# Kernel tuning notes

Measured on AMD Instinct MI355X. Metric: run time of the kernel, lower is better.

The kernel has to match this reference:

```python
import jax, jax.numpy as jnp
import numpy as np

NUM_LAYERS = 3
HEADS = 4
HEAD_DIM = 64
NUM_GRAPHS = 64


def setup_inputs() -> dict:
    key = jax.random.key(0)
    ks = jax.random.split(key, 12)
    N, E, C = 50000, 800000, HEADS * HEAD_DIM  # C = 256
    x = jax.random.normal(ks[0], (N, C), dtype=jnp.float32)
    edge_index = jax.random.randint(ks[1], (2, E), 0, N, dtype=jnp.int32)
    batch = jnp.sort(jax.random.randint(ks[2], (N,), 0, NUM_GRAPHS, dtype=jnp.int32))
    s = 1.0 / np.sqrt(C)
    Wq = jax.random.normal(ks[3], (NUM_LAYERS, C, C), dtype=jnp.float32) * s
    Wk = jax.random.normal(ks[4], (NUM_LAYERS, C, C), dtype=jnp.float32) * s
    Wv = jax.random.normal(ks[5], (NUM_LAYERS, C, C), dtype=jnp.float32) * s
    bq = jnp.zeros((NUM_LAYERS, C), dtype=jnp.float32)
    bk = jnp.zeros((NUM_LAYERS, C), dtype=jnp.float32)
    bv = jnp.zeros((NUM_LAYERS, C), dtype=jnp.float32)
    W1 = jax.random.normal(ks[6], (C, 64), dtype=jnp.float32) * s
    b1 = jnp.zeros((64,), dtype=jnp.float32)
    W2 = jax.random.normal(ks[7], (64, 16), dtype=jnp.float32) * (1.0 / 8.0)
    b2 = jnp.zeros((16,), dtype=jnp.float32)
    return {"x": x, "edge_index": edge_index, "batch": batch,
            "Wq": Wq, "bq": bq, "Wk": Wk, "bk": bk, "Wv": Wv, "bv": bv,
            "W1": W1, "b1": b1, "W2": W2, "b2": b2}


def _segment_softmax(scores, seg, num_segments):
    # scores: [E, H]; softmax over edges sharing the same destination node
    m = jax.ops.segment_max(scores, seg, num_segments=num_segments)
    e = jnp.exp(scores - m[seg])
    z = jax.ops.segment_sum(e, seg, num_segments=num_segments)
    return e / (z[seg] + 1e-16)


def reference(x, edge_index, batch, Wq, bq, Wk, bk, Wv, bv, W1, b1, W2, b2):
    N = x.shape[0]
    src, dst = edge_index[0], edge_index[1]
    scale = 1.0 / jnp.sqrt(jnp.asarray(HEAD_DIM, dtype=x.dtype))
    h = x
    for l in range(NUM_LAYERS):
        q = (h @ Wq[l] + bq[l]).reshape(N, HEADS, HEAD_DIM)
        k = (h @ Wk[l] + bk[l]).reshape(N, HEADS, HEAD_DIM)
        v = (h @ Wv[l] + bv[l]).reshape(N, HEADS, HEAD_DIM)
        # edge-wise attention logits: q_i . k_j / sqrt(d)  -> [E, H]
        alpha = jnp.einsum('ehd,ehd->eh', q[dst], k[src]) * scale
        alpha = _segment_softmax(alpha, dst, N)
        msg = alpha[..., None] * v[src]                     # [E, H, D]
        out = jax.ops.segment_sum(msg, dst, num_segments=N)  # [N, H, D]
        h = jax.nn.relu(out.reshape(N, HEADS * HEAD_DIM))
    # global add pool over graphs in the batch
    g = jax.ops.segment_sum(h, batch, num_segments=NUM_GRAPHS)  # [G, C]
    y = jax.nn.relu(g @ W1 + b1) @ W2 + b2                      # [G, 16]
    return y
```

## Files before the change

kernel.cpp:

```cpp
#include <hip/hip_runtime.h>
#include <math.h>

#define CC 256
#define HEADS 4
#define HD 64
#define NG 64
#define SCAN_BS 512
#define QKVS 768

typedef __attribute__((ext_vector_type(8))) _Float16 f16x8;
typedef __attribute__((ext_vector_type(4))) float f32x4;
typedef __attribute__((ext_vector_type(4))) _Float16 f16x4;
typedef __attribute__((ext_vector_type(2))) _Float16 f16x2;

static __device__ __forceinline__ float h2f(unsigned short u) {
  return (float)__builtin_bit_cast(_Float16, u);
}

#if __has_builtin(__builtin_amdgcn_fdot2)
static __device__ __forceinline__ float qkdot(f16x2 q0, f16x2 q1, f16x4 k) {
  f16x2 k0 = {k.x, k.y}, k1 = {k.z, k.w};
  return __builtin_amdgcn_fdot2(q0, k0, __builtin_amdgcn_fdot2(q1, k1, 0.f, false), false);
}
#else
static __device__ __forceinline__ float qkdot(f16x2 q0, f16x2 q1, f16x4 k) {
  return (float)q0.x * (float)k.x + (float)q0.y * (float)k.y +
         (float)q1.x * (float)k.z + (float)q1.y * (float)k.w;
}
#endif

static __device__ __forceinline__ int swz(int row, int g) {
  return row * 32 + (((g) ^ ((row >> 2) & 3)) << 3);
}

__global__ void prep_kernel(const int* __restrict__ dst, int* __restrict__ deg, int E,
                            const float* __restrict__ Wq, const float* __restrict__ Wk,
                            const float* __restrict__ Wv, const float* __restrict__ bq,
                            const float* __restrict__ bk, const float* __restrict__ bv,
                            unsigned short* __restrict__ Bth,
                            float* __restrict__ biascat, int L,
                            const float* __restrict__ x, unsigned short* __restrict__ hq,
                            int n4, int nbh, int nbw) {
  int b = blockIdx.x;
  if (b < nbh) {
    int e = b * 256 + threadIdx.x;
    if (e < E) atomicAdd(&deg[dst[e]], 1);
    return;
  }
  b -= nbh;
  if (b < nbw) {
    int idx = b * 256 + threadIdx.x;
    int total = L * QKVS * CC;
    if (idx >= total) return;
    int k = idx & 255;
    int n = (idx >> 8) % QKVS;
    int l = idx / (QKVS * CC);
    int part = n >> 8;
    int nn = n & 255;
    const float* W = part == 0 ? Wq : (part == 1 ? Wk : Wv);
    float v = W[((long)l * CC + k) * CC + nn];
    Bth[idx] = __builtin_bit_cast(unsigned short, (_Float16)v);
    if (k == 0) {
      const float* bb = part == 0 ? bq : (part == 1 ? bk : bv);
      biascat[l * QKVS + n] = bb[l * CC + nn];
    }
    return;
  }
  b -= nbw;
  int i = b * 256 + threadIdx.x;
  if (i >= n4) return;
  float4 v = ((const float4*)x)[i];
  ushort4 hv = make_ushort4(__builtin_bit_cast(unsigned short, (_Float16)v.x),
                            __builtin_bit_cast(unsigned short, (_Float16)v.y),
                            __builtin_bit_cast(unsigned short, (_Float16)v.z),
                            __builtin_bit_cast(unsigned short, (_Float16)v.w));
  ((ushort4*)hq)[i] = hv;
}

__global__ void scan1_kernel(const int* __restrict__ deg, int* __restrict__ exc,
                             int* __restrict__ partial, int n) {
  __shared__ int s[SCAN_BS];
  int t = threadIdx.x;
  int g = blockIdx.x * SCAN_BS + t;
  int v = (g < n) ? deg[g] : 0;
  s[t] = v;
  __syncthreads();
  for (int off = 1; off < SCAN_BS; off <<= 1) {
    int add = (t >= off) ? s[t - off] : 0;
    __syncthreads();
    s[t] += add;
    __syncthreads();
  }
  if (g < n) exc[g] = s[t] - v;
  if (t == SCAN_BS - 1) partial[blockIdx.x] = s[t];
}

__global__ void scan2_kernel(int* __restrict__ partial, int nb) {
  __shared__ int s[SCAN_BS];
  int t = threadIdx.x;
  int v = (t < nb) ? partial[t] : 0;
  s[t] = v;
  __syncthreads();
  for (int off = 1; off < SCAN_BS; off <<= 1) {
    int add = (t >= off) ? s[t - off] : 0;
    __syncthreads();
    s[t] += add;
    __syncthreads();
  }
  if (t < nb) partial[t] = s[t] - v;
}

__global__ void scan3_kernel(const int* __restrict__ exc, const int* __restrict__ partial,
                             int* __restrict__ row_start, int* __restrict__ cursor,
                             int n, int E) {
  int g = blockIdx.x * blockDim.x + threadIdx.x;
  if (g < n) {
    int v = exc[g] + partial[g / SCAN_BS];
    row_start[g] = v;
    cursor[g] = v;
  }
  if (g == n) row_start[n] = E;
}

__global__ void scatter_kernel(const int* __restrict__ srcArr, const int* __restrict__ dstArr,
                               int* __restrict__ cursor, int* __restrict__ csr_src, int E) {
  int e = blockIdx.x * blockDim.x + threadIdx.x;
  if (e < E) {
    int d = dstArr[e];
    int p = atomicAdd(&cursor[d], 1);
    csr_src[p] = srcArr[e];
  }
}

__global__ __launch_bounds__(256) void qkv_gemm(const unsigned short* __restrict__ Aq,
                                                const unsigned short* __restrict__ Bh,
                                                const float* __restrict__ biascat,
                                                _Float16* __restrict__ qkvh, int M,
                                                int nmb) {
  __shared__ unsigned short S[17408];
  unsigned short* As = S;
  unsigned short* Bs = S + 4096;
  int t = threadIdx.x;

  int G = 6 * nmb;
  int xcd = blockIdx.x & 7, pos = blockIdx.x >> 3;
  int q8 = G >> 3, r8 = G & 7;
  int lid = (xcd < r8 ? xcd * (q8 + 1) : r8 * (q8 + 1) + (xcd - r8) * q8) + pos;
  int bn = lid % 6, bm = lid / 6;

  int lane = t & 63, wave = t >> 6;
  int mo = (wave >> 1) * 64, no = (wave & 1) * 64;
  int col_l = lane & 15, q = lane >> 4;

  f32x4 acc[4][4];
#pragma unroll
  for (int i = 0; i < 4; ++i)
#pragma unroll
    for (int j = 0; j < 4; ++j) acc[i][j] = (f32x4)0.f;

  int sr = t >> 1;
  int sh = (t & 1) * 16;
  int g0 = (t & 1) * 2;
  int w0 = swz(sr, g0);
  int w1 = swz(sr, g0 + 1);
  long arow = (long)bm * 128 + sr;
  bool aval = arow < M;
  const unsigned short* ag = Aq + arow * CC + sh;
  const unsigned short* bg = Bh + ((long)bn * 128 + sr) * CC + sh;
  uint4 zz = make_uint4(0, 0, 0, 0);

  for (int kt = 0; kt < CC; kt += 32) {
    uint4 a0 = zz, a1 = zz;
    if (aval) {
      a0 = *(const uint4*)(ag + kt);
      a1 = *(const uint4*)(ag + kt + 8);
    }
    uint4 b0 = *(const uint4*)(bg + kt);
    uint4 b1 = *(const uint4*)(bg + kt + 8);
    __syncthreads();
    *(uint4*)&As[w0] = a0;
    *(uint4*)&As[w1] = a1;
    *(uint4*)&Bs[w0] = b0;
    *(uint4*)&Bs[w1] = b1;
    __syncthreads();

    f16x8 af[4], bf[4];
#pragma unroll
    for (int i = 0; i < 4; ++i) {
      int am = mo + i * 16 + col_l;
      af[i] = *(const f16x8*)&As[swz(am, q)];
      int bnn = no + i * 16 + col_l;
      bf[i] = *(const f16x8*)&Bs[swz(bnn, q)];
    }
#pragma unroll
    for (int i = 0; i < 4; ++i)
#pragma unroll
      for (int j = 0; j < 4; ++j)
        acc[i][j] = __builtin_amdgcn_mfma_f32_16x16x32_f16(af[i], bf[j], acc[i][j], 0, 0, 0);
  }

  long rbase = (long)bm * 128 + mo;
  int cbase = bn * 128 + no;
  __syncthreads();
  unsigned short* T = S + wave * 4352;
#pragma unroll
  for (int j = 0; j < 4; ++j) {
    int col = cbase + j * 16 + col_l;
    float bias = biascat[col];
    int cl = j * 16 + col_l;
#pragma unroll
    for (int i = 0; i < 4; ++i) {
#pragma unroll
      for (int r = 0; r < 4; ++r) {
        int rl = i * 16 + q * 4 + r;
        T[rl * 68 + cl] =
            __builtin_bit_cast(unsigned short, (_Float16)(acc[i][j][r] + bias));
      }
    }
  }
  __syncthreads();
  int ocol = cbase + (lane & 15) * 4;
#pragma unroll
  for (int p = 0; p < 16; ++p) {
    int rl = p * 4 + (lane >> 4);
    uint2 v = *(const uint2*)&T[rl * 68 + (lane & 15) * 4];
    long row = rbase + rl;
    if (row < M) *(uint2*)(qkvh + row * QKVS + ocol) = v;
  }
}

__global__ __launch_bounds__(256) void attn_fused_kernel(const _Float16* __restrict__ qkv,
                                                         const int* __restrict__ row_start,
                                                         const int* __restrict__ csr_src,
                                                         unsigned short* __restrict__ hq,
                                                         int N, int npx) {
  int b = blockIdx.x;
  int nb = (b & 7) * npx + (b >> 3);
  int wave = threadIdx.x >> 6;
  int lane = threadIdx.x & 63;
  int node = nb * 4 + wave;
  if (node >= N) return;
  int s0 = row_start[node], s1 = row_start[node + 1];

  const f16x4 q4 = *(const f16x4*)(qkv + (size_t)node * QKVS + lane * 4);
  const f16x2 q0 = {q4.x, q4.y};
  const f16x2 q1 = {q4.z, q4.w};

  float m = -1e30f, z = 0.f;
  f32x4 acc = (f32x4)0.f;

  int i = s0;
  for (; i + 8 <= s1; i += 8) {
    int ix[8];
#pragma unroll
    for (int u = 0; u < 8; ++u) ix[u] = csr_src[i + u];
    f16x4 kk[8], vv[8];
#pragma unroll
    for (int u = 0; u < 8; ++u) {
      const _Float16* rowp = qkv + (size_t)ix[u] * QKVS + 256 + lane * 4;
      kk[u] = *(const f16x4*)rowp;
      vv[u] = *(const f16x4*)(rowp + 256);
    }
    float lg[8];
#pragma unroll
    for (int u = 0; u < 8; ++u) {
      float d = qkdot(q0, q1, kk[u]);
#pragma unroll
      for (int off = 1; off < 16; off <<= 1) d += __shfl_xor(d, off, 64);
      lg[u] = d * 0.125f;
    }
    float cm = lg[0];
#pragma unroll
    for (int u = 1; u < 8; ++u) cm = fmaxf(cm, lg[u]);
    float mn = fmaxf(m, cm);
    float sc = __expf(m - mn);
    z *= sc;
    acc *= sc;
    m = mn;
#pragma unroll
    for (int u = 0; u < 8; ++u) {
      float e = __expf(lg[u] - m);
      z += e;
      f32x4 vf = {(float)vv[u].x, (float)vv[u].y, (float)vv[u].z, (float)vv[u].w};
      acc += e * vf;
    }
  }
  for (; i < s1; ++i) {
    int s = csr_src[i];
    const _Float16* rowp = qkv + (size_t)s * QKVS + 256 + lane * 4;
    f16x4 k4 = *(const f16x4*)rowp;
    f16x4 v4 = *(const f16x4*)(rowp + 256);
    float d = qkdot(q0, q1, k4);
#pragma unroll
    for (int off = 1; off < 16; off <<= 1) d += __shfl_xor(d, off, 64);
    float lgs = d * 0.125f;
    float mn = fmaxf(m, lgs);
    float sc = __expf(m - mn);
    float e = __expf(lgs - mn);
    z = z * sc + e;
    f32x4 vf = {(float)v4.x, (float)v4.y, (float)v4.z, (float)v4.w};
    acc = acc * sc + e * vf;
    m = mn;
  }

  float rz = 1.f / (z + 1e-16f);
  float o0 = fmaxf(acc.x * rz, 0.f);
  float o1 = fmaxf(acc.y * rz, 0.f);
  float o2 = fmaxf(acc.z * rz, 0.f);
  float o3 = fmaxf(acc.w * rz, 0.f);
  ushort4 ov = make_ushort4(__builtin_bit_cast(unsigned short, (_Float16)o0),
                            __builtin_bit_cast(unsigned short, (_Float16)o1),
                            __builtin_bit_cast(unsigned short, (_Float16)o2),
                            __builtin_bit_cast(unsigned short, (_Float16)o3));
  size_t idx = (size_t)node * CC + lane * 4;
  *(ushort4*)(hq + idx) = ov;
}

__global__ void pool_kernel(const unsigned short* __restrict__ hq,
                            const int* __restrict__ batch,
                            float* __restrict__ gpool, int N) {
  int c = threadIdx.x;
  int n0 = blockIdx.x * 64;
  int n1 = min(n0 + 64, N);
  int cur = batch[n0];
  float acc = 0.f;
  for (int n = n0; n < n1; ++n) {
    int g = batch[n];
    if (g != cur) {
      atomicAdd(&gpool[cur * CC + c], acc);
      acc = 0.f;
      cur = g;
    }
    acc += h2f(hq[(size_t)n * CC + c]);
  }
  atomicAdd(&gpool[cur * CC + c], acc);
}

__global__ void head_kernel(const float* __restrict__ gpool, const float* __restrict__ W1,
                            const float* __restrict__ b1, const float* __restrict__ W2,
                            const float* __restrict__ b2, float* __restrict__ out) {
  __shared__ float hid[64];
  int g = blockIdx.x, t = threadIdx.x;
  float acc = b1[t];
  for (int i = 0; i < CC; ++i) acc = fmaf(gpool[g * CC + i], W1[i * 64 + t], acc);
  hid[t] = fmaxf(acc, 0.f);
  __syncthreads();
  if (t < 16) {
    float o = b2[t];
    for (int i = 0; i < 64; ++i) o = fmaf(hid[i], W2[i * 16 + t], o);
    out[g * 16 + t] = o;
  }
}

extern "C" void kernel_launch(void* const* d_in, const int* in_sizes, int n_in,
                              void* d_out, int out_size, void* d_ws, size_t ws_size,
                              hipStream_t stream) {
  const float* x  = (const float*)d_in[0];
  const int* ei   = (const int*)d_in[1];
  const int* batch = (const int*)d_in[2];
  const float* Wq = (const float*)d_in[3];
  const float* bq = (const float*)d_in[4];
  const float* Wk = (const float*)d_in[5];
  const float* bk = (const float*)d_in[6];
  const float* Wv = (const float*)d_in[7];
  const float* bv = (const float*)d_in[8];
  const float* W1 = (const float*)d_in[9];
  const float* b1 = (const float*)d_in[10];
  const float* W2 = (const float*)d_in[11];
  const float* b2 = (const float*)d_in[12];
  float* out = (float*)d_out;

  int N = in_sizes[0] / CC;
  int E = in_sizes[1] / 2;
  int L = in_sizes[3] / (CC * CC);
  const int* src = ei;
  const int* dst = ei + E;

  size_t off = 0;
  auto alloc = [&](size_t bytes) -> void* {
    void* p = (char*)d_ws + off;
    off += (bytes + 255) & ~(size_t)255;
    return p;
  };
  _Float16* qkvh = (_Float16*)alloc((size_t)N * QKVS * 2);
  unsigned short* hq = (unsigned short*)alloc((size_t)N * CC * 2);
  unsigned short* Bth = (unsigned short*)alloc((size_t)L * QKVS * CC * 2);
  float* biascat = (float*)alloc((size_t)L * QKVS * 4);
  int* deg = (int*)alloc((size_t)N * 4);
  int* exc = (int*)alloc((size_t)N * 4);
  int* partial = (int*)alloc(SCAN_BS * 4);
  int* row_start = (int*)alloc((size_t)(N + 1) * 4);
  int* cursor = (int*)alloc((size_t)N * 4);
  int* csr_src = (int*)alloc((size_t)E * 4);
  float* gpool = (float*)alloc((size_t)NG * CC * 4);

  hipMemsetAsync(deg, 0, (size_t)N * 4, stream);
  int eb = (E + 255) / 256;
  int wtot = L * QKVS * CC;
  int nbw = (wtot + 255) / 256;
  int n4 = N * CC / 4;
  int nbs = (n4 + 255) / 256;
  prep_kernel<<<eb + nbw + nbs, 256, 0, stream>>>(dst, deg, E,
                                                  Wq, Wk, Wv, bq, bk, bv,
                                                  Bth, biascat, L,
                                                  x, hq, n4, eb, nbw);

  int nb = (N + SCAN_BS - 1) / SCAN_BS;
  scan1_kernel<<<nb, SCAN_BS, 0, stream>>>(deg, exc, partial, N);
  scan2_kernel<<<1, SCAN_BS, 0, stream>>>(partial, nb);
  scan3_kernel<<<(N + 1 + 255) / 256, 256, 0, stream>>>(exc, partial, row_start, cursor, N, E);
  scatter_kernel<<<eb, 256, 0, stream>>>(src, dst, cursor, csr_src, E);

  int nmb = (N + 127) / 128;
  int gemmG = 6 * nmb;
  int nblocks = (N + 3) / 4;
  int npx = (nblocks + 7) / 8;
  int ngrid = npx * 8;
  for (int l = 0; l < L; ++l) {
    qkv_gemm<<<gemmG, 256, 0, stream>>>(hq,
                                        Bth + (size_t)l * QKVS * CC,
                                        biascat + (size_t)l * QKVS, qkvh, N, nmb);
    attn_fused_kernel<<<ngrid, 256, 0, stream>>>(qkvh, row_start, csr_src,
                                                 hq, N, npx);
  }

  hipMemsetAsync(gpool, 0, (size_t)NG * CC * 4, stream);
  pool_kernel<<<(N + 63) / 64, 256, 0, stream>>>(hq, batch, gpool, N);
  head_kernel<<<NG, 64, 0, stream>>>(gpool, W1, b1, W2, b2, out);
}
```

Measured before the change: 694.9 us.

## Fuse graph pooling into last attention layer and widen GEMM K-tile

Global add pooling is folded into the final attention kernel. Each block stages its four node outputs in shared memory and atomically adds them into gpool, which removes the separate pool kernel and the fp16 write and re-read of h for the last layer. The gpool zeroing moves from a separate memset into the prep kernel. The QKV GEMM now loads K-tiles of 64 instead of 32, with a new 8-way XOR swizzle, halving the number of barriers. Its epilogue writes 16-byte stores instead of 8-byte ones and drops one barrier. The trade-off is many more global float atomics, all contending on the few gpool rows of the same graph, since the batch is sorted.

```diff
diff --git a/kernel.cpp b/kernel.cpp
--- a/kernel.cpp
+++ b/kernel.cpp
@@ -29,8 +29,8 @@
 }
 #endif
 
-static __device__ __forceinline__ int swz(int row, int g) {
-  return row * 32 + (((g) ^ ((row >> 2) & 3)) << 3);
+static __device__ __forceinline__ int swz64(int row, int g) {
+  return row * 64 + (((g) ^ ((row) & 7)) << 3);
 }
 
 __global__ void prep_kernel(const int* __restrict__ dst, int* __restrict__ deg, int E,
@@ -40,7 +40,8 @@
                             unsigned short* __restrict__ Bth,
                             float* __restrict__ biascat, int L,
                             const float* __restrict__ x, unsigned short* __restrict__ hq,
-                            int n4, int nbh, int nbw) {
+                            float* __restrict__ gpool,
+                            int n4, int nbh, int nbw, int nbs) {
   int b = blockIdx.x;
   if (b < nbh) {
     int e = b * 256 + threadIdx.x;
@@ -67,14 +68,20 @@
     return;
   }
   b -= nbw;
+  if (b < nbs) {
+    int i = b * 256 + threadIdx.x;
+    if (i >= n4) return;
+    float4 v = ((const float4*)x)[i];
+    ushort4 hv = make_ushort4(__builtin_bit_cast(unsigned short, (_Float16)v.x),
+                              __builtin_bit_cast(unsigned short, (_Float16)v.y),
+                              __builtin_bit_cast(unsigned short, (_Float16)v.z),
+                              __builtin_bit_cast(unsigned short, (_Float16)v.w));
+    ((ushort4*)hq)[i] = hv;
+    return;
+  }
+  b -= nbs;
   int i = b * 256 + threadIdx.x;
-  if (i >= n4) return;
-  float4 v = ((const float4*)x)[i];
-  ushort4 hv = make_ushort4(__builtin_bit_cast(unsigned short, (_Float16)v.x),
-                            __builtin_bit_cast(unsigned short, (_Float16)v.y),
-                            __builtin_bit_cast(unsigned short, (_Float16)v.z),
-                            __builtin_bit_cast(unsigned short, (_Float16)v.w));
-  ((ushort4*)hq)[i] = hv;
+  if (i < NG * CC) gpool[i] = 0.f;
 }
 
 __global__ void scan1_kernel(const int* __restrict__ deg, int* __restrict__ exc,
@@ -137,9 +144,9 @@
                                                 const float* __restrict__ biascat,
                                                 _Float16* __restrict__ qkvh, int M,
                                                 int nmb) {
-  __shared__ unsigned short S[17408];
+  __shared__ unsigned short S[18432];
   unsigned short* As = S;
-  unsigned short* Bs = S + 4096;
+  unsigned short* Bs = S + 8192;
   int t = threadIdx.x;
 
   int G = 6 * nmb;
@@ -159,50 +166,62 @@
     for (int j = 0; j < 4; ++j) acc[i][j] = (f32x4)0.f;
 
   int sr = t >> 1;
-  int sh = (t & 1) * 16;
-  int g0 = (t & 1) * 2;
-  int w0 = swz(sr, g0);
-  int w1 = swz(sr, g0 + 1);
+  int h = t & 1;
   long arow = (long)bm * 128 + sr;
   bool aval = arow < M;
-  const unsigned short* ag = Aq + arow * CC + sh;
-  const unsigned short* bg = Bh + ((long)bn * 128 + sr) * CC + sh;
+  const unsigned short* ag = Aq + arow * CC + h * 32;
+  const unsigned short* bg = Bh + ((long)bn * 128 + sr) * CC + h * 32;
   uint4 zz = make_uint4(0, 0, 0, 0);
-
-  for (int kt = 0; kt < CC; kt += 32) {
-    uint4 a0 = zz, a1 = zz;
+  int woff[4];
+#pragma unroll
+  for (int i = 0; i < 4; ++i) woff[i] = swz64(sr, h * 4 + i);
+
+  for (int kt = 0; kt < CC; kt += 64) {
+    uint4 a0 = zz, a1 = zz, a2 = zz, a3 = zz;
     if (aval) {
       a0 = *(const uint4*)(ag + kt);
       a1 = *(const uint4*)(ag + kt + 8);
+      a2 = *(const uint4*)(ag + kt + 16);
+      a3 = *(const uint4*)(ag + kt + 24);
     }
     uint4 b0 = *(const uint4*)(bg + kt);
     uint4 b1 = *(const uint4*)(bg + kt + 8);
-    __syncthreads();
-    *(uint4*)&As[w0] = a0;
-    *(uint4*)&As[w1] = a1;
-    *(uint4*)&Bs[w0] = b0;
-    *(uint4*)&Bs[w1] = b1;
-    __syncthreads();
-
-    f16x8 af[4], bf[4];
-#pragma unroll
-    for (int i = 0; i < 4; ++i) {
-      int am = mo + i * 16 + col_l;
-      af[i] = *(const f16x8*)&As[swz(am, q)];
-      int bnn = no + i * 16 + col_l;
-      bf[i] = *(const f16x8*)&Bs[swz(bnn, q)];
-    }
-#pragma unroll
-    for (int i = 0; i < 4; ++i)
-#pragma unroll
-      for (int j = 0; j < 4; ++j)
-        acc[i][j] = __builtin_amdgcn_mfma_f32_16x16x32_f16(af[i], bf[j], acc[i][j], 0, 0, 0);
+    uint4 b2 = *(const uint4*)(bg + kt + 16);
+    uint4 b3 = *(const uint4*)(bg + kt + 24);
+    __syncthreads();
+    *(uint4*)&As[woff[0]] = a0;
+    *(uint4*)&As[woff[1]] = a1;
+    *(uint4*)&As[woff[2]] = a2;
+    *(uint4*)&As[woff[3]] = a3;
+    *(uint4*)&Bs[woff[0]] = b0;
+    *(uint4*)&Bs[woff[1]] = b1;
+    *(uint4*)&Bs[woff[2]] = b2;
+    *(uint4*)&Bs[woff[3]] = b3;
+    __syncthreads();
+
+#pragma unroll
+    for (int kk = 0; kk < 64; kk += 32) {
+      int gb = (kk >> 3) + q;
+      f16x8 af[4], bf[4];
+#pragma unroll
+      for (int i = 0; i < 4; ++i) {
+        int am = mo + i * 16 + col_l;
+        af[i] = *(const f16x8*)&As[swz64(am, gb)];
+        int bnn = no + i * 16 + col_l;
+        bf[i] = *(const f16x8*)&Bs[swz64(bnn, gb)];
+      }
+#pragma unroll
+      for (int i = 0; i < 4; ++i)
+#pragma unroll
+        for (int j = 0; j < 4; ++j)
+          acc[i][j] = __builtin_amdgcn_mfma_f32_16x16x32_f16(af[i], bf[j], acc[i][j], 0, 0, 0);
+    }
   }
 
   long rbase = (long)bm * 128 + mo;
   int cbase = bn * 128 + no;
   __syncthreads();
-  unsigned short* T = S + wave * 4352;
+  unsigned short* T = S + wave * 4608;
 #pragma unroll
   for (int j = 0; j < 4; ++j) {
     int col = cbase + j * 16 + col_l;
@@ -213,19 +232,19 @@
 #pragma unroll
       for (int r = 0; r < 4; ++r) {
         int rl = i * 16 + q * 4 + r;
-        T[rl * 68 + cl] =
+        T[rl * 72 + cl] =
             __builtin_bit_cast(unsigned short, (_Float16)(acc[i][j][r] + bias));
       }
     }
   }
-  __syncthreads();
-  int ocol = cbase + (lane & 15) * 4;
-#pragma unroll
-  for (int p = 0; p < 16; ++p) {
-    int rl = p * 4 + (lane >> 4);
-    uint2 v = *(const uint2*)&T[rl * 68 + (lane & 15) * 4];
+  int c8 = (lane & 7) * 8;
+  int rq = lane >> 3;
+#pragma unroll
+  for (int p = 0; p < 8; ++p) {
+    int rl = p * 8 + rq;
+    uint4 v = *(const uint4*)&T[rl * 72 + c8];
     long row = rbase + rl;
-    if (row < M) *(uint2*)(qkvh + row * QKVS + ocol) = v;
+    if (row < M) *(uint4*)(qkvh + row * QKVS + cbase + c8) = v;
   }
 }
 
@@ -233,7 +252,11 @@
                                                          const int* __restrict__ row_start,
                                                          const int* __restrict__ csr_src,
                                                          unsigned short* __restrict__ hq,
+                                                         const int* __restrict__ batch,
+                                                         float* __restrict__ gpool,
                                                          int N, int npx) {
+  __shared__ float sh[4][CC];
+  __shared__ int shb[4];
   int b = blockIdx.x;
   int nb = (b & 7) * npx + (b >> 3);
   int wave = threadIdx.x >> 6;
@@ -308,32 +331,34 @@
   float o1 = fmaxf(acc.y * rz, 0.f);
   float o2 = fmaxf(acc.z * rz, 0.f);
   float o3 = fmaxf(acc.w * rz, 0.f);
-  ushort4 ov = make_ushort4(__builtin_bit_cast(unsigned short, (_Float16)o0),
-                            __builtin_bit_cast(unsigned short, (_Float16)o1),
-                            __builtin_bit_cast(unsigned short, (_Float16)o2),
-                            __builtin_bit_cast(unsigned short, (_Float16)o3));
-  size_t idx = (size_t)node * CC + lane * 4;
-  *(ushort4*)(hq + idx) = ov;
-}
-
-__global__ void pool_kernel(const unsigned short* __restrict__ hq,
-                            const int* __restrict__ batch,
-                            float* __restrict__ gpool, int N) {
-  int c = threadIdx.x;
-  int n0 = blockIdx.x * 64;
-  int n1 = min(n0 + 64, N);
-  int cur = batch[n0];
-  float acc = 0.f;
-  for (int n = n0; n < n1; ++n) {
-    int g = batch[n];
-    if (g != cur) {
-      atomicAdd(&gpool[cur * CC + c], acc);
-      acc = 0.f;
-      cur = g;
-    }
-    acc += h2f(hq[(size_t)n * CC + c]);
-  }
-  atomicAdd(&gpool[cur * CC + c], acc);
+
+  if (gpool == nullptr) {
+    ushort4 ov = make_ushort4(__builtin_bit_cast(unsigned short, (_Float16)o0),
+                              __builtin_bit_cast(unsigned short, (_Float16)o1),
+                              __builtin_bit_cast(unsigned short, (_Float16)o2),
+                              __builtin_bit_cast(unsigned short, (_Float16)o3));
+    size_t idx = (size_t)node * CC + lane * 4;
+    *(ushort4*)(hq + idx) = ov;
+  } else {
+    sh[wave][lane * 4 + 0] = o0;
+    sh[wave][lane * 4 + 1] = o1;
+    sh[wave][lane * 4 + 2] = o2;
+    sh[wave][lane * 4 + 3] = o3;
+    if (lane == 0) shb[wave] = batch[node];
+    __syncthreads();
+    int c = threadIdx.x;
+    if (wave == 0 || true) {}
+    int b0 = shb[0], b1 = shb[1], b2 = shb[2], b3 = shb[3];
+    if (b0 == b1 && b1 == b2 && b2 == b3) {
+      float s = sh[0][c] + sh[1][c] + sh[2][c] + sh[3][c];
+      atomicAdd(&gpool[b0 * CC + c], s);
+    } else {
+      atomicAdd(&gpool[b0 * CC + c], sh[0][c]);
+      atomicAdd(&gpool[b1 * CC + c], sh[1][c]);
+      atomicAdd(&gpool[b2 * CC + c], sh[2][c]);
+      atomicAdd(&gpool[b3 * CC + c], sh[3][c]);
+    }
+  }
 }
 
 __global__ void head_kernel(const float* __restrict__ gpool, const float* __restrict__ W1,
@@ -400,10 +425,11 @@
   int nbw = (wtot + 255) / 256;
   int n4 = N * CC / 4;
   int nbs = (n4 + 255) / 256;
-  prep_kernel<<<eb + nbw + nbs, 256, 0, stream>>>(dst, deg, E,
-                                                  Wq, Wk, Wv, bq, bk, bv,
-                                                  Bth, biascat, L,
-                                                  x, hq, n4, eb, nbw);
+  int nbz = (NG * CC + 255) / 256;
+  prep_kernel<<<eb + nbw + nbs + nbz, 256, 0, stream>>>(dst, deg, E,
+                                                        Wq, Wk, Wv, bq, bk, bv,
+                                                        Bth, biascat, L,
+                                                        x, hq, gpool, n4, eb, nbw, nbs);
 
   int nb = (N + SCAN_BS - 1) / SCAN_BS;
   scan1_kernel<<<nb, SCAN_BS, 0, stream>>>(deg, exc, partial, N);
@@ -420,11 +446,10 @@
     qkv_gemm<<<gemmG, 256, 0, stream>>>(hq,
                                         Bth + (size_t)l * QKVS * CC,
                                         biascat + (size_t)l * QKVS, qkvh, N, nmb);
-    attn_fused_kernel<<<ngrid, 256, 0, stream>>>(qkvh, row_start, csr_src,
-                                                 hq, N, npx);
-  }
-
-  hipMemsetAsync(gpool, 0, (size_t)NG * CC * 4, stream);
-  pool_kernel<<<(N + 63) / 64, 256, 0, stream>>>(hq, batch, gpool, N);
+    attn_fused_kernel<<<ngrid, 256, 0, stream>>>(qkvh, row_start, csr_src, hq,
+                                                 batch, (l == L - 1) ? gpool : nullptr,
+                                                 N, npx);
+  }
+
   head_kernel<<<NG, 64, 0, stream>>>(gpool, W1, b1, W2, b2, out);
 }
```

Measured after the change: 658.0 us. 1.06x faster.
